# Optimization experiments

Hardware: AMD Instinct MI355X
Metric: run time of the kernel (lower is better)

Reference implementation:

```python
import jax, jax.numpy as jnp
import numpy as np

K = 12
ORDERS = [(1, 2, 3), (1, 3, 2), (3, 2, 1), (3, 1, 2), (2, 1, 3), (2, 3, 1)]


def ranking_3d(x):
    # x: (B, L1, W1, H1, D) -> (B, 12, L1*W1*H1, D)
    B, L1, W1, H1, D = x.shape
    seqs = []
    for dims in ORDERS:
        perm = (0,) + dims + (4,)
        seqs.append(jnp.transpose(x, perm).reshape(B, -1, D))
        xr = jnp.flip(x, axis=dims)
        seqs.append(jnp.transpose(xr, perm).reshape(B, -1, D))
    return jnp.stack(seqs, axis=1)


def restore_original(out_y, shape):
    # out_y: (B, 12, D, L). NOTE: faithfully replicates the original code, which
    # reshapes the (B, D, L) slice directly to (B, d1, d2, d3, D).
    B, L1, W1, H1, D = shape
    size = {1: L1, 2: W1, 3: H1}
    restored = []
    for i in range(12):
        dims = ORDERS[i // 2]
        seq = out_y[:, i]  # (B, D, L)
        dims_shape = tuple(size[d] for d in dims)
        reshaped = seq.reshape((B,) + dims_shape + (D,))
        perm = (0,) + dims + (4,)
        inv = tuple(np.argsort(perm))
        r = jnp.transpose(reshaped, inv)
        if i % 2 == 1:
            r = jnp.flip(r, axis=dims)
        restored.append(r)
    return restored


def selective_scan(u, delta, A, Bs, Cs):
    # u, delta: (B,K,D,L); A: (K,D,N); Bs, Cs: (B,K,N,L)
    us = jnp.moveaxis(u, -1, 0)       # (L,B,K,D)
    ds = jnp.moveaxis(delta, -1, 0)   # (L,B,K,D)
    Bts = jnp.moveaxis(Bs, -1, 0)     # (L,B,K,N)
    Cts = jnp.moveaxis(Cs, -1, 0)     # (L,B,K,N)
    h0 = jnp.zeros(u.shape[:-1] + (A.shape[-1],), u.dtype)  # (B,K,D,N)

    def step(h, inp):
        ut, dt, Bt, Ct = inp
        dA = jnp.exp(dt[..., None] * A)                       # (B,K,D,N)
        h = dA * h + (dt * ut)[..., None] * Bt[:, :, None, :]
        y = jnp.einsum('bkdn,bkn->bkd', h, Ct)
        return h, y

    _, ys = jax.lax.scan(step, h0, (us, ds, Bts, Cts))
    return jnp.moveaxis(ys, 0, -1)  # (B,K,D,L)


def setup_inputs() -> dict:
    key = jax.random.key(0)
    ks = jax.random.split(key, 8)
    B, H, W, Len, D = 1, 16, 16, 16, 128
    N, R = 16, 8
    x = jax.random.normal(ks[0], (B, H, W, Len, D), dtype=jnp.float32)
    x_proj_weight = jax.random.normal(ks[1], (K, R + 2 * N, D), dtype=jnp.float32) * 0.02
    std = R ** -0.5
    dt_projs_weight = jax.random.uniform(ks[2], (K, D, R), minval=-std, maxval=std, dtype=jnp.float32)
    dt = jnp.exp(jax.random.uniform(ks[3], (K, D)) * (np.log(0.1) - np.log(0.001)) + np.log(0.001))
    dt = jnp.clip(dt, 1e-4, None)
    dt_projs_bias = (dt + jnp.log(-jnp.expm1(-dt))).astype(jnp.float32)
    A_logs = jnp.broadcast_to(jnp.log(jnp.arange(1, N + 1, dtype=jnp.float32)), (K, D, N)).copy()
    Ds = jnp.ones((K, D), dtype=jnp.float32)
    merge_w = jax.random.normal(ks[4], (K,), dtype=jnp.float32) * (1.0 / K)
    merge_b = jax.random.normal(ks[5], (), dtype=jnp.float32) * 0.01
    return {'x': x, 'x_proj_weight': x_proj_weight, 'dt_projs_weight': dt_projs_weight,
            'dt_projs_bias': dt_projs_bias, 'A_logs': A_logs, 'Ds': Ds,
            'merge_w': merge_w, 'merge_b': merge_b}


def reference(x, x_proj_weight, dt_projs_weight, dt_projs_bias, A_logs, Ds, merge_w, merge_b):
    B, H, W, Len, D = x.shape
    L = H * W * Len
    R = dt_projs_weight.shape[-1]
    N = A_logs.shape[-1]
    xs = jnp.transpose(ranking_3d(x), (0, 1, 3, 2))  # (B,K,D,L)
    x_dbl = jnp.einsum('bkdl,kcd->bkcl', xs, x_proj_weight)  # (B,K,R+2N,L)
    dts, Bs, Cs = jnp.split(x_dbl, [R, R + N], axis=2)
    dts = jnp.einsum('bkrl,kdr->bkdl', dts, dt_projs_weight)
    delta = jax.nn.softplus(dts + dt_projs_bias[None, :, :, None])
    A = -jnp.exp(A_logs)  # (K,D,N)
    ys = selective_scan(xs, delta, A, Bs, Cs)
    out_y = ys + Ds[None, :, :, None] * xs  # (B,K,D,L)
    restored = restore_original(out_y, (B, H, W, Len, D))
    stacked = jnp.stack(restored, axis=1)  # (B,K,H,W,Len,D)
    # mergeconv: 1x1 Conv2d over K channels == weighted sum across directions
    y = jnp.einsum('bkhwld,k->bhwld', stacked, merge_w) + merge_b
    return y
```

## Files before the change

kernel.cpp:

```cpp
#include <hip/hip_runtime.h>

#define KK 12
#define LL 4096
#define DD 128
#define NN 16
#define RR 8
#define NC 256
#define LCS 16
#define LB 32
#define XST 140
#define SDST 44

__device__ __forceinline__ int pos_of(int k, int l) {
    int o = k >> 1;
    int le = (k & 1) ? (4095 - l) : l;
    int t1 = le >> 8, t2 = (le >> 4) & 15, t3 = le & 15;
    switch (o) {
        case 0:  return (t1 << 8) | (t2 << 4) | t3;
        case 1:  return (t1 << 8) | (t3 << 4) | t2;
        case 2:  return (t3 << 8) | (t2 << 4) | t1;
        case 3:  return (t2 << 8) | (t3 << 4) | t1;
        case 4:  return (t2 << 8) | (t1 << 4) | t3;
        default: return (t3 << 8) | (t1 << 4) | t2;
    }
}

__device__ __forceinline__ unsigned pk_bf2(float a, float b) {
    unsigned ua = __float_as_uint(a); ua = (ua + 0x7FFF + ((ua >> 16) & 1)) >> 16;
    unsigned ub = __float_as_uint(b); ub = (ub + 0x7FFF + ((ub >> 16) & 1)) >> 16;
    return ua | (ub << 16);
}
__device__ __forceinline__ float lo_bf(unsigned u) { return __uint_as_float(u << 16); }
__device__ __forceinline__ float hi_bf(unsigned u) { return __uint_as_float(u & 0xFFFF0000u); }

__device__ __forceinline__ float delta_row_z(const float* sdbl, int l,
                                             float4 w0, float4 w1, float bz) {
    const float4* dr = (const float4*)(sdbl + l * SDST);
    float4 r0 = dr[0], r1 = dr[1];
    return bz + w0.x * r0.x + w0.y * r0.y + w0.z * r0.z + w0.w * r0.w
              + w1.x * r1.x + w1.y * r1.y + w1.z * r1.z + w1.w * r1.w;
}

__device__ __forceinline__ bool load_A16(const float* __restrict__ A_logs,
                                         int k, int d, float* A16) {
    const float4* ap = (const float4*)(A_logs + (size_t)(k * DD + d) * NN);
    #pragma unroll
    for (int q = 0; q < 4; q++) {
        float4 a4 = ap[q];
        A16[4*q+0] = -__expf(a4.x); A16[4*q+1] = -__expf(a4.y);
        A16[4*q+2] = -__expf(a4.z); A16[4*q+3] = -__expf(a4.w);
    }
    bool s = true;
    #pragma unroll
    for (int j = 1; j < 16; j++) {
        float m = (float)(j + 1);
        s = s && (fabsf(A16[j] - m * A16[0]) <= 1e-4f * m * fabsf(A16[0]));
    }
    return s;
}

__device__ __forceinline__ void e16_tree(float q, float* e) {
    e[0] = q;
    float q2 = q * q;
    e[1] = q2; e[2] = q2 * q; e[3] = q2 * q2;
    e[4] = e[3] * q;   e[5] = e[3] * q2;  e[6] = e[3] * e[2];  e[7] = e[3] * e[3];
    e[8] = e[7] * q;   e[9] = e[7] * q2;  e[10] = e[7] * e[2]; e[11] = e[7] * e[3];
    e[12] = e[7] * e[4]; e[13] = e[7] * e[5]; e[14] = e[7] * e[6]; e[15] = e[7] * e[7];
}

template<bool S>
__device__ __forceinline__ void e16_from(float v, const float* A16, float* e) {
    if (S) {
        e16_tree(__expf(v * A16[0]), e);
    } else {
        #pragma unroll
        for (int j = 0; j < 16; j++) e[j] = __expf(v * A16[j]);
    }
}

template<bool S>
__device__ __forceinline__ void scanA_body(
    float* xs, const float* sdbl, int k, int cc, int lbase, int d,
    const float* A16, float4 w0, float4 w1, float bz, float Dval,
    unsigned* __restrict__ S_b, float* __restrict__ dtsum,
    float* __restrict__ dslp)
{
    float h[16];
    #pragma unroll
    for (int n = 0; n < 16; n++) h[n] = 0.0f;
    float dsum = 0.0f;

    #pragma unroll 4
    for (int i = 0; i < LCS; i++) {
        int l = lbase + i;
        float z = delta_row_z(sdbl, l, w0, w1, bz);
        float E = __expf(-fabsf(z));
        float dt = fmaxf(z, 0.0f) + __logf(1.0f + E);
        float u = xs[l * XST + d];
        dsum += dt;
        dslp[(size_t)i * DD] = dsum;
        float tu = dt * u;
        float e[16];
        e16_from<S>(dt, A16, e);
        const float4* bp = (const float4*)(&sdbl[l * SDST + 8]);
        float4 b0 = bp[0], b1 = bp[1], b2 = bp[2], b3 = bp[3];
        const float4* cp = (const float4*)(&sdbl[l * SDST + 24]);
        float4 c0 = cp[0], c1 = cp[1], c2 = cp[2], c3 = cp[3];
        h[0]  = e[0]  * h[0]  + tu * b0.x;  h[1]  = e[1]  * h[1]  + tu * b0.y;
        h[2]  = e[2]  * h[2]  + tu * b0.z;  h[3]  = e[3]  * h[3]  + tu * b0.w;
        h[4]  = e[4]  * h[4]  + tu * b1.x;  h[5]  = e[5]  * h[5]  + tu * b1.y;
        h[6]  = e[6]  * h[6]  + tu * b1.z;  h[7]  = e[7]  * h[7]  + tu * b1.w;
        h[8]  = e[8]  * h[8]  + tu * b2.x;  h[9]  = e[9]  * h[9]  + tu * b2.y;
        h[10] = e[10] * h[10] + tu * b2.z;  h[11] = e[11] * h[11] + tu * b2.w;
        h[12] = e[12] * h[12] + tu * b3.x;  h[13] = e[13] * h[13] + tu * b3.y;
        h[14] = e[14] * h[14] + tu * b3.z;  h[15] = e[15] * h[15] + tu * b3.w;
        float y = h[0]*c0.x + h[1]*c0.y + h[2]*c0.z + h[3]*c0.w
                + h[4]*c1.x + h[5]*c1.y + h[6]*c1.z + h[7]*c1.w
                + h[8]*c2.x + h[9]*c2.y + h[10]*c2.z + h[11]*c2.w
                + h[12]*c3.x + h[13]*c3.y + h[14]*c3.z + h[15]*c3.w;
        xs[l * XST + d] = y + Dval * u;
    }

    size_t b8 = ((size_t)(k * NC + cc) * DD + d) * 8;
    uint4 p0, p1;
    p0.x = pk_bf2(h[0],  h[1]);  p0.y = pk_bf2(h[2],  h[3]);
    p0.z = pk_bf2(h[4],  h[5]);  p0.w = pk_bf2(h[6],  h[7]);
    p1.x = pk_bf2(h[8],  h[9]);  p1.y = pk_bf2(h[10], h[11]);
    p1.z = pk_bf2(h[12], h[13]); p1.w = pk_bf2(h[14], h[15]);
    *(uint4*)(S_b + b8)     = p0;
    *(uint4*)(S_b + b8 + 4) = p1;
    dtsum[(k * NC + cc) * DD + d] = dsum;
}

__global__ __launch_bounds__(256, 4) void k1_proj_scanA(
    const float* __restrict__ x, const float* __restrict__ Wp,
    const float* __restrict__ Wdt, const float* __restrict__ bias,
    const float* __restrict__ A_logs, const float* __restrict__ Ds,
    unsigned* __restrict__ S_b, float* __restrict__ dtsum,
    float* __restrict__ oy, float* __restrict__ csp,
    float* __restrict__ dsl)
{
    const int blk = blockIdx.x;
    const int k = blk >> 7;
    const int c = blk & 127;
    const int l0 = c * LB;
    const int t = threadIdx.x;

    __shared__ __align__(16) float xs[LB * XST];
    __shared__ __align__(16) float sdbl[LB * SDST];
    __shared__ int pos_s[LB];

    if (t < LB) pos_s[t] = pos_of(k, l0 + t);
    __syncthreads();

    {
        int lane32 = t & 31, rowi = t >> 5;
        #pragma unroll
        for (int p = 0; p < 4; p++) {
            int l = p * 8 + rowi;
            float4 v = *(const float4*)(x + (size_t)pos_s[l] * DD + lane32 * 4);
            *(float4*)(&xs[l * XST + lane32 * 4]) = v;
        }
    }
    __syncthreads();

    {
        int l = t & 31, cg = t >> 5;
        float acc[5];
        #pragma unroll
        for (int j = 0; j < 5; j++) acc[j] = 0.0f;
        const float* wk = Wp + (size_t)(k * 40 + cg * 5) * DD;
        for (int d4 = 0; d4 < DD; d4 += 4) {
            float4 xv = *(const float4*)(&xs[l * XST + d4]);
            #pragma unroll
            for (int j = 0; j < 5; j++) {
                const float* w = wk + j * DD + d4;
                acc[j] += xv.x * w[0] + xv.y * w[1] + xv.z * w[2] + xv.w * w[3];
            }
        }
        #pragma unroll
        for (int j = 0; j < 5; j++) sdbl[l * SDST + cg * 5 + j] = acc[j];
    }
    __syncthreads();

    {
        float4* g4 = (float4*)(csp + (size_t)blk * 512);
        for (int idx = t; idx < 128; idx += 256) {
            int l = idx >> 2, q = idx & 3;
            g4[idx] = *(const float4*)(&sdbl[l * SDST + 24 + q * 4]);
        }
    }

    const int d = t & 127, half = t >> 7;
    const int cc = 2 * c + half, lbase = half * LCS;
    float A16[16];
    bool structured = load_A16(A_logs, k, d, A16);
    const float4* wp4 = (const float4*)(Wdt + (size_t)(k * DD + d) * RR);
    const float4 w0 = wp4[0], w1 = wp4[1];
    const float bz = bias[k * DD + d];
    const float Dval = Ds[k * DD + d];
    float* dslp = dsl + ((size_t)(k * LL + l0 + lbase)) * DD + d;

    if (structured)
        scanA_body<true>(xs, sdbl, k, cc, lbase, d, A16, w0, w1, bz, Dval,
                         S_b, dtsum, dslp);
    else
        scanA_body<false>(xs, sdbl, k, cc, lbase, d, A16, w0, w1, bz, Dval,
                          S_b, dtsum, dslp);

    {
        float* base = oy + ((size_t)(k * DD + d)) * LL + l0 + lbase;
        #pragma unroll
        for (int p = 0; p < 4; p++) {
            int j = p * 4;
            float4 v = make_float4(xs[(lbase + j + 0) * XST + d],
                                   xs[(lbase + j + 1) * XST + d],
                                   xs[(lbase + j + 2) * XST + d],
                                   xs[(lbase + j + 3) * XST + d]);
            *(float4*)(base + j) = v;
        }
    }
}

__global__ __launch_bounds__(256) void k2_combine(
    unsigned* __restrict__ S_b, const float* __restrict__ dtsum,
    const float* __restrict__ A_logs)
{
    int tid = blockIdx.x * 256 + threadIdx.x;
    int kk = tid >> 10, rem = tid & 1023, dd2 = rem >> 3, j = rem & 7;
    const float* ap = A_logs + ((size_t)kk * DD + dd2) * NN + 2 * j;
    float A0 = -__expf(ap[0]), A1 = -__expf(ap[1]);
    float h0 = 0.0f, h1 = 0.0f;
    #pragma unroll 8
    for (int c2 = 0; c2 < NC; c2++) {
        size_t b8 = ((size_t)(kk * NC + c2) * DD + dd2) * 8 + j;
        unsigned u = S_b[b8];
        float dsv = dtsum[(kk * NC + c2) * DD + dd2];
        float s0 = lo_bf(u), s1 = hi_bf(u);
        S_b[b8] = pk_bf2(h0, h1);
        h0 = s0 + __expf(dsv * A0) * h0;
        h1 = s1 + __expf(dsv * A1) * h1;
    }
}

template<bool S>
__device__ __forceinline__ void corr_body(
    float* ybuf, const float* csp_s, const float* dslp, int lbase, int d,
    const float* A16, const float* g)
{
    #pragma unroll 4
    for (int i = 0; i < LCS; i++) {
        int l = lbase + i;
        float Dsum = dslp[(size_t)i * DD];
        float e[16];
        e16_from<S>(Dsum, A16, e);
        const float4* cp = (const float4*)(&csp_s[l * 16]);
        float4 c0 = cp[0], c1 = cp[1], c2 = cp[2], c3 = cp[3];
        float y = e[0]*g[0]*c0.x + e[1]*g[1]*c0.y + e[2]*g[2]*c0.z + e[3]*g[3]*c0.w
                + e[4]*g[4]*c1.x + e[5]*g[5]*c1.y + e[6]*g[6]*c1.z + e[7]*g[7]*c1.w
                + e[8]*g[8]*c2.x + e[9]*g[9]*c2.y + e[10]*g[10]*c2.z + e[11]*g[11]*c2.w
                + e[12]*g[12]*c3.x + e[13]*g[13]*c3.y + e[14]*g[14]*c3.z + e[15]*g[15]*c3.w;
        ybuf[l * XST + d] = y;
    }
}

__global__ __launch_bounds__(256, 4) void k3_corr(
    const float* __restrict__ A_logs, const unsigned* __restrict__ S_b,
    const float* __restrict__ csp, const float* __restrict__ dsl,
    float* __restrict__ oy)
{
    const int blk = blockIdx.x;
    const int k = blk >> 7;
    const int c = blk & 127;
    const int l0 = c * LB;
    const int t = threadIdx.x;

    __shared__ __align__(16) float csp_s[LB * 16];
    __shared__ __align__(16) float ybuf[LB * XST];
    {
        const float4* g4 = (const float4*)(csp + (size_t)blk * 512);
        float4* s4 = (float4*)csp_s;
        for (int idx = t; idx < 128; idx += 256) s4[idx] = g4[idx];
    }
    __syncthreads();

    const int d = t & 127, half = t >> 7;
    const int cc = 2 * c + half, lbase = half * LCS;
    float A16[16];
    bool structured = load_A16(A_logs, k, d, A16);
    const float* dslp = dsl + ((size_t)(k * LL + l0 + lbase)) * DD + d;

    float g[16];
    {
        const uint4* hp = (const uint4*)(S_b + ((size_t)(k * NC + cc) * DD + d) * 8);
        uint4 a = hp[0], b = hp[1];
        g[0]  = lo_bf(a.x); g[1]  = hi_bf(a.x); g[2]  = lo_bf(a.y); g[3]  = hi_bf(a.y);
        g[4]  = lo_bf(a.z); g[5]  = hi_bf(a.z); g[6]  = lo_bf(a.w); g[7]  = hi_bf(a.w);
        g[8]  = lo_bf(b.x); g[9]  = hi_bf(b.x); g[10] = lo_bf(b.y); g[11] = hi_bf(b.y);
        g[12] = lo_bf(b.z); g[13] = hi_bf(b.z); g[14] = lo_bf(b.w); g[15] = hi_bf(b.w);
    }

    if (structured)
        corr_body<true>(ybuf, csp_s, dslp, lbase, d, A16, g);
    else
        corr_body<false>(ybuf, csp_s, dslp, lbase, d, A16, g);

    {
        float* base = oy + ((size_t)(k * DD + d)) * LL + l0 + lbase;
        #pragma unroll
        for (int p = 0; p < 4; p++) {
            int j = p * 4;
            float4 v = *(float4*)(base + j);
            v.x += ybuf[(lbase + j + 0) * XST + d];
            v.y += ybuf[(lbase + j + 1) * XST + d];
            v.z += ybuf[(lbase + j + 2) * XST + d];
            v.w += ybuf[(lbase + j + 3) * XST + d];
            *(float4*)(base + j) = v;
        }
    }
}

__global__ __launch_bounds__(256) void k4_merge(
    const float* __restrict__ out_y, const float* __restrict__ mw,
    const float* __restrict__ mb, float* __restrict__ out)
{
    int idx = blockIdx.x * 256 + threadIdx.x;
    int dd = idx & 127;
    int p = idx >> 7;
    int i3 = p & 15, i2 = (p >> 4) & 15, i1 = (p >> 8) & 15;

    float accv = mb[0];
    #pragma unroll
    for (int k = 0; k < 12; k++) {
        int a1 = i1, a2 = i2, a3 = i3;
        if (k & 1) { a1 = 15 - i1; a2 = 15 - i2; a3 = 15 - i3; }
        int j1, j2, j3;
        switch (k >> 1) {
            case 0:  j1 = a1; j2 = a2; j3 = a3; break;
            case 1:  j1 = a1; j2 = a3; j3 = a2; break;
            case 2:  j1 = a3; j2 = a2; j3 = a1; break;
            case 3:  j1 = a3; j2 = a1; j3 = a2; break;
            case 4:  j1 = a2; j2 = a1; j3 = a3; break;
            default: j1 = a2; j2 = a3; j3 = a1; break;
        }
        int jb = (j1 << 8) | (j2 << 4) | j3;
        accv += mw[k] * out_y[(size_t)k * (DD * LL) + (jb >> 5) * LL
                              + ((jb & 31) << 7) + dd];
    }
    out[idx] = accv;
}

extern "C" void kernel_launch(void* const* d_in, const int* in_sizes, int n_in,
                              void* d_out, int out_size, void* d_ws, size_t ws_size,
                              hipStream_t stream) {
    const float* x      = (const float*)d_in[0];
    const float* Wp     = (const float*)d_in[1];
    const float* Wdt    = (const float*)d_in[2];
    const float* bias   = (const float*)d_in[3];
    const float* A_logs = (const float*)d_in[4];
    const float* Ds     = (const float*)d_in[5];
    const float* mw     = (const float*)d_in[6];
    const float* mb     = (const float*)d_in[7];
    float* out = (float*)d_out;

    unsigned* S_b = (unsigned*)d_ws;
    float* dts  = (float*)(S_b + (size_t)KK * NC * DD * 8);
    float* oy   = dts + (size_t)KK * NC * DD;
    float* csp  = oy + (size_t)KK * DD * LL;
    float* dsl  = csp + (size_t)KK * 128 * 512;

    k1_proj_scanA<<<dim3(KK * 128), dim3(256), 0, stream>>>(
        x, Wp, Wdt, bias, A_logs, Ds, S_b, dts, oy, csp, dsl);
    k2_combine<<<dim3(KK * DD * 8 / 256), dim3(256), 0, stream>>>(S_b, dts, A_logs);
    k3_corr<<<dim3(KK * 128), dim3(256), 0, stream>>>(A_logs, S_b, csp, dsl, oy);
    k4_merge<<<dim3(LL * DD / 256), dim3(256), 0, stream>>>(oy, mw, mb, out);
}
```

Before: 171.5 us.

## Write scan outputs in restored order so merge reads contiguous float4 rows

The scan and correction kernels now write each direction's output straight into the restored spatial order, using an inverse position map and float4 stores from registers. This removes the shared-memory staging buffers and lets the merge kernel do a plain vectorized weighted sum over 12 contiguous planes instead of gathering. A small pre-kernel computes -exp(A_logs) once so the scan kernels load it instead of recomputing it. The trade-off is an extra launch and global stores that are scattered per thread in k1 and k3.

```diff
diff --git a/kernel.cpp b/kernel.cpp
--- a/kernel.cpp
+++ b/kernel.cpp
@@ -25,6 +25,21 @@
     }
 }
 
+__device__ __forceinline__ int inv_pos(int k, int jb) {
+    int j1 = jb >> 8, j2 = (jb >> 4) & 15, j3 = jb & 15;
+    int a1, a2, a3;
+    switch (k >> 1) {
+        case 0:  a1 = j1; a2 = j2; a3 = j3; break;
+        case 1:  a1 = j1; a3 = j2; a2 = j3; break;
+        case 2:  a3 = j1; a2 = j2; a1 = j3; break;
+        case 3:  a3 = j1; a1 = j2; a2 = j3; break;
+        case 4:  a2 = j1; a1 = j2; a3 = j3; break;
+        default: a2 = j1; a3 = j2; a1 = j3; break;
+    }
+    if (k & 1) { a1 = 15 - a1; a2 = 15 - a2; a3 = 15 - a3; }
+    return (a1 << 8) | (a2 << 4) | a3;
+}
+
 __device__ __forceinline__ unsigned pk_bf2(float a, float b) {
     unsigned ua = __float_as_uint(a); ua = (ua + 0x7FFF + ((ua >> 16) & 1)) >> 16;
     unsigned ub = __float_as_uint(b); ub = (ub + 0x7FFF + ((ub >> 16) & 1)) >> 16;
@@ -41,14 +56,13 @@
               + w1.x * r1.x + w1.y * r1.y + w1.z * r1.z + w1.w * r1.w;
 }
 
-__device__ __forceinline__ bool load_A16(const float* __restrict__ A_logs,
-                                         int k, int d, float* A16) {
-    const float4* ap = (const float4*)(A_logs + (size_t)(k * DD + d) * NN);
+__device__ __forceinline__ bool load_negA16(const float* __restrict__ negA,
+                                            int k, int d, float* A16) {
+    const float4* ap = (const float4*)(negA + (size_t)(k * DD + d) * NN);
     #pragma unroll
     for (int q = 0; q < 4; q++) {
         float4 a4 = ap[q];
-        A16[4*q+0] = -__expf(a4.x); A16[4*q+1] = -__expf(a4.y);
-        A16[4*q+2] = -__expf(a4.z); A16[4*q+3] = -__expf(a4.w);
+        A16[4*q+0] = a4.x; A16[4*q+1] = a4.y; A16[4*q+2] = a4.z; A16[4*q+3] = a4.w;
     }
     bool s = true;
     #pragma unroll
@@ -78,17 +92,25 @@
     }
 }
 
+__global__ __launch_bounds__(256) void k0_negA(
+    const float* __restrict__ A_logs, float* __restrict__ negA)
+{
+    int idx = blockIdx.x * 256 + threadIdx.x;
+    negA[idx] = -__expf(A_logs[idx]);
+}
+
 template<bool S>
 __device__ __forceinline__ void scanA_body(
-    float* xs, const float* sdbl, int k, int cc, int lbase, int d,
+    const float* xs, const float* sdbl, int k, int cc, int lbase, int d,
     const float* A16, float4 w0, float4 w1, float bz, float Dval,
     unsigned* __restrict__ S_b, float* __restrict__ dtsum,
-    float* __restrict__ dslp)
+    float* __restrict__ dslp, float* __restrict__ obase)
 {
     float h[16];
     #pragma unroll
     for (int n = 0; n < 16; n++) h[n] = 0.0f;
     float dsum = 0.0f;
+    float4 yv4;
 
     #pragma unroll 4
     for (int i = 0; i < LCS; i++) {
@@ -118,7 +140,12 @@
                 + h[4]*c1.x + h[5]*c1.y + h[6]*c1.z + h[7]*c1.w
                 + h[8]*c2.x + h[9]*c2.y + h[10]*c2.z + h[11]*c2.w
                 + h[12]*c3.x + h[13]*c3.y + h[14]*c3.z + h[15]*c3.w;
-        xs[l * XST + d] = y + Dval * u;
+        y += Dval * u;
+        int ph = i & 3;
+        if (ph == 0) yv4.x = y;
+        else if (ph == 1) yv4.y = y;
+        else if (ph == 2) yv4.z = y;
+        else { yv4.w = y; *(float4*)(obase + (i & ~3)) = yv4; }
     }
 
     size_t b8 = ((size_t)(k * NC + cc) * DD + d) * 8;
@@ -135,9 +162,9 @@
 __global__ __launch_bounds__(256, 4) void k1_proj_scanA(
     const float* __restrict__ x, const float* __restrict__ Wp,
     const float* __restrict__ Wdt, const float* __restrict__ bias,
-    const float* __restrict__ A_logs, const float* __restrict__ Ds,
+    const float* __restrict__ negA, const float* __restrict__ Ds,
     unsigned* __restrict__ S_b, float* __restrict__ dtsum,
-    float* __restrict__ oy, float* __restrict__ csp,
+    float* __restrict__ oy2, float* __restrict__ csp,
     float* __restrict__ dsl)
 {
     const int blk = blockIdx.x;
@@ -194,42 +221,33 @@
     const int d = t & 127, half = t >> 7;
     const int cc = 2 * c + half, lbase = half * LCS;
     float A16[16];
-    bool structured = load_A16(A_logs, k, d, A16);
+    bool structured = load_negA16(negA, k, d, A16);
     const float4* wp4 = (const float4*)(Wdt + (size_t)(k * DD + d) * RR);
     const float4 w0 = wp4[0], w1 = wp4[1];
     const float bz = bias[k * DD + d];
     const float Dval = Ds[k * DD + d];
     float* dslp = dsl + ((size_t)(k * LL + l0 + lbase)) * DD + d;
 
+    int jb = (d << 5) | (c >> 2);
+    int p = inv_pos(k, jb);
+    float* obase = oy2 + (size_t)k * (LL * DD) + (p << 7) + (c & 3) * 32 + lbase;
+
     if (structured)
         scanA_body<true>(xs, sdbl, k, cc, lbase, d, A16, w0, w1, bz, Dval,
-                         S_b, dtsum, dslp);
+                         S_b, dtsum, dslp, obase);
     else
         scanA_body<false>(xs, sdbl, k, cc, lbase, d, A16, w0, w1, bz, Dval,
-                          S_b, dtsum, dslp);
-
-    {
-        float* base = oy + ((size_t)(k * DD + d)) * LL + l0 + lbase;
-        #pragma unroll
-        for (int p = 0; p < 4; p++) {
-            int j = p * 4;
-            float4 v = make_float4(xs[(lbase + j + 0) * XST + d],
-                                   xs[(lbase + j + 1) * XST + d],
-                                   xs[(lbase + j + 2) * XST + d],
-                                   xs[(lbase + j + 3) * XST + d]);
-            *(float4*)(base + j) = v;
-        }
-    }
+                          S_b, dtsum, dslp, obase);
 }
 
 __global__ __launch_bounds__(256) void k2_combine(
     unsigned* __restrict__ S_b, const float* __restrict__ dtsum,
-    const float* __restrict__ A_logs)
+    const float* __restrict__ negA)
 {
     int tid = blockIdx.x * 256 + threadIdx.x;
     int kk = tid >> 10, rem = tid & 1023, dd2 = rem >> 3, j = rem & 7;
-    const float* ap = A_logs + ((size_t)kk * DD + dd2) * NN + 2 * j;
-    float A0 = -__expf(ap[0]), A1 = -__expf(ap[1]);
+    const float* ap = negA + ((size_t)kk * DD + dd2) * NN + 2 * j;
+    float A0 = ap[0], A1 = ap[1];
     float h0 = 0.0f, h1 = 0.0f;
     #pragma unroll 8
     for (int c2 = 0; c2 < NC; c2++) {
@@ -245,29 +263,38 @@
 
 template<bool S>
 __device__ __forceinline__ void corr_body(
-    float* ybuf, const float* csp_s, const float* dslp, int lbase, int d,
-    const float* A16, const float* g)
-{
-    #pragma unroll 4
-    for (int i = 0; i < LCS; i++) {
-        int l = lbase + i;
-        float Dsum = dslp[(size_t)i * DD];
-        float e[16];
-        e16_from<S>(Dsum, A16, e);
-        const float4* cp = (const float4*)(&csp_s[l * 16]);
-        float4 c0 = cp[0], c1 = cp[1], c2 = cp[2], c3 = cp[3];
-        float y = e[0]*g[0]*c0.x + e[1]*g[1]*c0.y + e[2]*g[2]*c0.z + e[3]*g[3]*c0.w
-                + e[4]*g[4]*c1.x + e[5]*g[5]*c1.y + e[6]*g[6]*c1.z + e[7]*g[7]*c1.w
-                + e[8]*g[8]*c2.x + e[9]*g[9]*c2.y + e[10]*g[10]*c2.z + e[11]*g[11]*c2.w
-                + e[12]*g[12]*c3.x + e[13]*g[13]*c3.y + e[14]*g[14]*c3.z + e[15]*g[15]*c3.w;
-        ybuf[l * XST + d] = y;
+    const float* csp_s, const float* dslp, int lbase, int d,
+    const float* A16, const float* g, float* __restrict__ obase)
+{
+    #pragma unroll
+    for (int q4 = 0; q4 < 4; q4++) {
+        float v0, v1, v2, v3;
+        #pragma unroll
+        for (int j = 0; j < 4; j++) {
+            int i = q4 * 4 + j;
+            int l = lbase + i;
+            float Dsum = dslp[(size_t)i * DD];
+            float e[16];
+            e16_from<S>(Dsum, A16, e);
+            const float4* cp = (const float4*)(&csp_s[l * 16]);
+            float4 c0 = cp[0], c1 = cp[1], c2 = cp[2], c3 = cp[3];
+            float y = e[0]*g[0]*c0.x + e[1]*g[1]*c0.y + e[2]*g[2]*c0.z + e[3]*g[3]*c0.w
+                    + e[4]*g[4]*c1.x + e[5]*g[5]*c1.y + e[6]*g[6]*c1.z + e[7]*g[7]*c1.w
+                    + e[8]*g[8]*c2.x + e[9]*g[9]*c2.y + e[10]*g[10]*c2.z + e[11]*g[11]*c2.w
+                    + e[12]*g[12]*c3.x + e[13]*g[13]*c3.y + e[14]*g[14]*c3.z + e[15]*g[15]*c3.w;
+            if (j == 0) v0 = y; else if (j == 1) v1 = y;
+            else if (j == 2) v2 = y; else v3 = y;
+        }
+        float4 o = *(float4*)(obase + q4 * 4);
+        o.x += v0; o.y += v1; o.z += v2; o.w += v3;
+        *(float4*)(obase + q4 * 4) = o;
     }
 }
 
 __global__ __launch_bounds__(256, 4) void k3_corr(
-    const float* __restrict__ A_logs, const unsigned* __restrict__ S_b,
+    const float* __restrict__ negA, const unsigned* __restrict__ S_b,
     const float* __restrict__ csp, const float* __restrict__ dsl,
-    float* __restrict__ oy)
+    float* __restrict__ oy2)
 {
     const int blk = blockIdx.x;
     const int k = blk >> 7;
@@ -276,7 +303,6 @@
     const int t = threadIdx.x;
 
     __shared__ __align__(16) float csp_s[LB * 16];
-    __shared__ __align__(16) float ybuf[LB * XST];
     {
         const float4* g4 = (const float4*)(csp + (size_t)blk * 512);
         float4* s4 = (float4*)csp_s;
@@ -287,7 +313,7 @@
     const int d = t & 127, half = t >> 7;
     const int cc = 2 * c + half, lbase = half * LCS;
     float A16[16];
-    bool structured = load_A16(A_logs, k, d, A16);
+    bool structured = load_negA16(negA, k, d, A16);
     const float* dslp = dsl + ((size_t)(k * LL + l0 + lbase)) * DD + d;
 
     float g[16];
@@ -300,54 +326,31 @@
         g[12] = lo_bf(b.z); g[13] = hi_bf(b.z); g[14] = lo_bf(b.w); g[15] = hi_bf(b.w);
     }
 
+    int jb = (d << 5) | (c >> 2);
+    int p = inv_pos(k, jb);
+    float* obase = oy2 + (size_t)k * (LL * DD) + (p << 7) + (c & 3) * 32 + lbase;
+
     if (structured)
-        corr_body<true>(ybuf, csp_s, dslp, lbase, d, A16, g);
+        corr_body<true>(csp_s, dslp, lbase, d, A16, g, obase);
     else
-        corr_body<false>(ybuf, csp_s, dslp, lbase, d, A16, g);
-
-    {
-        float* base = oy + ((size_t)(k * DD + d)) * LL + l0 + lbase;
-        #pragma unroll
-        for (int p = 0; p < 4; p++) {
-            int j = p * 4;
-            float4 v = *(float4*)(base + j);
-            v.x += ybuf[(lbase + j + 0) * XST + d];
-            v.y += ybuf[(lbase + j + 1) * XST + d];
-            v.z += ybuf[(lbase + j + 2) * XST + d];
-            v.w += ybuf[(lbase + j + 3) * XST + d];
-            *(float4*)(base + j) = v;
-        }
-    }
+        corr_body<false>(csp_s, dslp, lbase, d, A16, g, obase);
 }
 
 __global__ __launch_bounds__(256) void k4_merge(
-    const float* __restrict__ out_y, const float* __restrict__ mw,
+    const float* __restrict__ oy2, const float* __restrict__ mw,
     const float* __restrict__ mb, float* __restrict__ out)
 {
     int idx = blockIdx.x * 256 + threadIdx.x;
-    int dd = idx & 127;
-    int p = idx >> 7;
-    int i3 = p & 15, i2 = (p >> 4) & 15, i1 = (p >> 8) & 15;
-
-    float accv = mb[0];
+    const float4* src = (const float4*)oy2;
+    float b = mb[0];
+    float4 acc = make_float4(b, b, b, b);
     #pragma unroll
     for (int k = 0; k < 12; k++) {
-        int a1 = i1, a2 = i2, a3 = i3;
-        if (k & 1) { a1 = 15 - i1; a2 = 15 - i2; a3 = 15 - i3; }
-        int j1, j2, j3;
-        switch (k >> 1) {
-            case 0:  j1 = a1; j2 = a2; j3 = a3; break;
-            case 1:  j1 = a1; j2 = a3; j3 = a2; break;
-            case 2:  j1 = a3; j2 = a2; j3 = a1; break;
-            case 3:  j1 = a3; j2 = a1; j3 = a2; break;
-            case 4:  j1 = a2; j2 = a1; j3 = a3; break;
-            default: j1 = a2; j2 = a3; j3 = a1; break;
-        }
-        int jb = (j1 << 8) | (j2 << 4) | j3;
-        accv += mw[k] * out_y[(size_t)k * (DD * LL) + (jb >> 5) * LL
-                              + ((jb & 31) << 7) + dd];
-    }
-    out[idx] = accv;
+        float4 v = src[(size_t)k * (LL * DD / 4) + idx];
+        float w = mw[k];
+        acc.x += w * v.x; acc.y += w * v.y; acc.z += w * v.z; acc.w += w * v.w;
+    }
+    ((float4*)out)[idx] = acc;
 }
 
 extern "C" void kernel_launch(void* const* d_in, const int* in_sizes, int n_in,
@@ -365,13 +368,15 @@
 
     unsigned* S_b = (unsigned*)d_ws;
     float* dts  = (float*)(S_b + (size_t)KK * NC * DD * 8);
-    float* oy   = dts + (size_t)KK * NC * DD;
-    float* csp  = oy + (size_t)KK * DD * LL;
+    float* oy2  = dts + (size_t)KK * NC * DD;
+    float* csp  = oy2 + (size_t)KK * DD * LL;
     float* dsl  = csp + (size_t)KK * 128 * 512;
-
+    float* negA = dsl + (size_t)KK * LL * DD;
+
+    k0_negA<<<dim3(KK * DD * NN / 256), dim3(256), 0, stream>>>(A_logs, negA);
     k1_proj_scanA<<<dim3(KK * 128), dim3(256), 0, stream>>>(
-        x, Wp, Wdt, bias, A_logs, Ds, S_b, dts, oy, csp, dsl);
-    k2_combine<<<dim3(KK * DD * 8 / 256), dim3(256), 0, stream>>>(S_b, dts, A_logs);
-    k3_corr<<<dim3(KK * 128), dim3(256), 0, stream>>>(A_logs, S_b, csp, dsl, oy);
-    k4_merge<<<dim3(LL * DD / 256), dim3(256), 0, stream>>>(oy, mw, mb, out);
-}
+        x, Wp, Wdt, bias, negA, Ds, S_b, dts, oy2, csp, dsl);
+    k2_combine<<<dim3(KK * DD * 8 / 256), dim3(256), 0, stream>>>(S_b, dts, negA);
+    k3_corr<<<dim3(KK * 128), dim3(256), 0, stream>>>(negA, S_b, csp, dsl, oy2);
+    k4_merge<<<dim3(LL * DD / 4 / 256), dim3(256), 0, stream>>>(oy2, mw, mb, out);
+}
```

Result: slower. 181.2 us (+5.6%).
